# Optimization experiments

Measured on AMD Instinct MI355X. Metric: run time of the kernel, lower is better.

Reference implementation:

```python
import jax, jax.numpy as jnp
import numpy as np

N = 100000
E = 800000
D_IN, D_H, D_OUT = 128, 128, 128


def setup_inputs() -> dict:
    key = jax.random.key(0)
    ks = jax.random.split(key, 8)
    x = jax.random.normal(ks[0], (N, D_IN), dtype=jnp.float32)
    edge_index = jax.random.randint(ks[1], (2, E), 0, N, dtype=jnp.int64)
    s = 1.0 / np.sqrt(D_IN)
    W1 = jax.random.uniform(ks[2], (D_H, D_IN), minval=-s, maxval=s, dtype=jnp.float32)
    b1 = jax.random.uniform(ks[3], (D_H,), minval=-s, maxval=s, dtype=jnp.float32)
    sh = 1.0 / np.sqrt(D_H)
    W2 = jax.random.uniform(ks[4], (D_H, D_H), minval=-sh, maxval=sh, dtype=jnp.float32)
    b2 = jax.random.uniform(ks[5], (D_H,), minval=-sh, maxval=sh, dtype=jnp.float32)
    W3 = jax.random.uniform(ks[6], (D_OUT, D_H), minval=-sh, maxval=sh, dtype=jnp.float32)
    b3 = jax.random.uniform(ks[7], (D_OUT,), minval=-sh, maxval=sh, dtype=jnp.float32)
    return {"x": x, "edge_index": edge_index, "W1": W1, "b1": b1,
            "W2": W2, "b2": b2, "W3": W3, "b3": b3}


def reference(x, edge_index, W1, b1, W2, b2, W3, b3):
    row, col = edge_index[0], edge_index[1]
    n = x.shape[0]
    # in-degree of destination nodes (bincount over row), clamped to 1
    deg = jnp.clip(
        jax.ops.segment_sum(jnp.ones_like(row, dtype=x.dtype), row, num_segments=n),
        1.0)  # [N]

    def mp(h):
        # gather messages from source nodes, scatter-add to destinations, mean, relu
        agg = jax.ops.segment_sum(h[col], row, num_segments=n)  # [N, d]
        return jax.nn.relu(agg / deg[:, None])

    h = mp(x @ W1.T + b1)
    h = mp(h @ W2.T + b2)
    return h @ W3.T + b3
```

## Files before the change

kernel.cpp:

```cpp
#include <hip/hip_runtime.h>

#define NNODES 100000
#define NEDGES 800000
#define D 128
#define NB1 391


__global__ __launch_bounds__(256) void k_count(const int* __restrict__ ei,
                                               int* __restrict__ cnt) {
    int e = blockIdx.x * 256 + threadIdx.x;
    atomicAdd(&cnt[ei[e]], 1);
}

__global__ __launch_bounds__(256) void k_scan1(const int* __restrict__ cnt,
                                               int* __restrict__ off,
                                               int* __restrict__ bsum) {
    __shared__ int s[256];
    int t = threadIdx.x;
    int i = blockIdx.x * 256 + t;
    int v = (i < NNODES) ? cnt[i] : 0;
    s[t] = v;
    __syncthreads();
    for (int d = 1; d < 256; d <<= 1) {
        int a = (t >= d) ? s[t - d] : 0;
        __syncthreads();
        s[t] += a;
        __syncthreads();
    }
    if (i < NNODES) off[i] = s[t] - v;
    if (t == 255) bsum[blockIdx.x] = s[255];
}

__global__ __launch_bounds__(512) void k_scan2(int* __restrict__ bsum) {
    __shared__ int s[512];
    int t = threadIdx.x;
    int v = (t < NB1) ? bsum[t] : 0;
    s[t] = v;
    __syncthreads();
    for (int d = 1; d < 512; d <<= 1) {
        int a = (t >= d) ? s[t - d] : 0;
        __syncthreads();
        s[t] += a;
        __syncthreads();
    }
    if (t < NB1) bsum[t] = s[t] - v;
}

__global__ __launch_bounds__(256) void k_scan3(int* __restrict__ off,
                                               const int* __restrict__ bsum,
                                               int* __restrict__ cur) {
    int i = blockIdx.x * 256 + threadIdx.x;
    if (i < NNODES) {
        int o = off[i] + bsum[blockIdx.x];
        off[i] = o;
        cur[i] = o;
    }
}

__global__ __launch_bounds__(256) void k_fill(const int* __restrict__ ei,
                                              int* __restrict__ cur,
                                              int* __restrict__ csr) {
    int e = blockIdx.x * 256 + threadIdx.x;
    int r = ei[e];
    int c = ei[NEDGES + e];
    int p = atomicAdd(&cur[r], 1);
    csr[p] = c;
}


static __device__ __forceinline__ void fma4(float4& acc, float s, const float4& v) {
    acc.x = fmaf(s, v.x, acc.x);
    acc.y = fmaf(s, v.y, acc.y);
    acc.z = fmaf(s, v.z, acc.z);
    acc.w = fmaf(s, v.w, acc.w);
}

static __device__ __forceinline__ int swz(int j, int k) {
    return (k << 7) + ((((j >> 2) ^ (k & 31)) << 2) | (j & 3));
}

__global__ __launch_bounds__(512, 4) void k_gemm(const float* __restrict__ in,
                                                 const float* __restrict__ W,
                                                 const float* __restrict__ bias,
                                                 float* __restrict__ out) {
    __shared__ float Wt[D * D];
    int t = threadIdx.x;
#pragma unroll
    for (int it = 0; it < 8; ++it) {
        int e4 = it * 512 + t;
        float4 w = ((const float4*)W)[e4];
        int e = e4 * 4;
        int j = e >> 7, k = e & 127;
        Wt[swz(j, k + 0)] = w.x;
        Wt[swz(j, k + 1)] = w.y;
        Wt[swz(j, k + 2)] = w.z;
        Wt[swz(j, k + 3)] = w.w;
    }
    int jl = t & 31;
    int ng = t >> 5;
    int j0 = jl * 4;
    float4 b4 = *(const float4*)(bias + j0);
    __syncthreads();

    int nb = blockIdx.x * 64 + ng * 4;
    if (nb >= NNODES) return;
    const float* p0 = in + (size_t)(nb + 0) * D;
    const float* p1 = in + (size_t)(nb + 1) * D;
    const float* p2 = in + (size_t)(nb + 2) * D;
    const float* p3 = in + (size_t)(nb + 3) * D;
    float4 a0 = b4, a1 = b4, a2 = b4, a3 = b4;
#pragma unroll 4
    for (int k = 0; k < D; k += 4) {
        const float4 w0 = *(const float4*)(Wt + swz(j0, k + 0));
        const float4 w1 = *(const float4*)(Wt + swz(j0, k + 1));
        const float4 w2 = *(const float4*)(Wt + swz(j0, k + 2));
        const float4 w3 = *(const float4*)(Wt + swz(j0, k + 3));
        float4 x0 = *(const float4*)(p0 + k);
        float4 x1 = *(const float4*)(p1 + k);
        float4 x2 = *(const float4*)(p2 + k);
        float4 x3 = *(const float4*)(p3 + k);
        fma4(a0, x0.x, w0); fma4(a0, x0.y, w1); fma4(a0, x0.z, w2); fma4(a0, x0.w, w3);
        fma4(a1, x1.x, w0); fma4(a1, x1.y, w1); fma4(a1, x1.z, w2); fma4(a1, x1.w, w3);
        fma4(a2, x2.x, w0); fma4(a2, x2.y, w1); fma4(a2, x2.z, w2); fma4(a2, x2.w, w3);
        fma4(a3, x3.x, w0); fma4(a3, x3.y, w1); fma4(a3, x3.z, w2); fma4(a3, x3.w, w3);
    }
    *(float4*)(out + (size_t)(nb + 0) * D + j0) = a0;
    *(float4*)(out + (size_t)(nb + 1) * D + j0) = a1;
    *(float4*)(out + (size_t)(nb + 2) * D + j0) = a2;
    *(float4*)(out + (size_t)(nb + 3) * D + j0) = a3;
}


__global__ __launch_bounds__(256) void k_mp(const float* __restrict__ h,
                                            const int* __restrict__ off,
                                            const int* __restrict__ cnt,
                                            const int* __restrict__ csr,
                                            float* __restrict__ agg) {
    int gid = blockIdx.x * 256 + threadIdx.x;
    int node = gid >> 6;
    int lane = threadIdx.x & 63;
    if (node >= NNODES) return;
    int begin = off[node];
    int c = cnt[node];
    float ax = 0.f, ay = 0.f;
    for (int e = 0; e < c; ++e) {
        int src = csr[begin + e];
        float2 v = *(const float2*)(h + (size_t)src * D + lane * 2);
        ax += v.x;
        ay += v.y;
    }
    float inv = 1.0f / fmaxf((float)c, 1.0f);
    float2 r;
    r.x = fmaxf(ax * inv, 0.f);
    r.y = fmaxf(ay * inv, 0.f);
    *(float2*)(agg + (size_t)node * D + lane * 2) = r;
}


extern "C" void kernel_launch(void* const* d_in, const int* in_sizes, int n_in,
                              void* d_out, int out_size, void* d_ws, size_t ws_size,
                              hipStream_t stream) {
    const float* x  = (const float*)d_in[0];
    const int*   ei = (const int*)d_in[1];
    const float* W1 = (const float*)d_in[2];
    const float* b1 = (const float*)d_in[3];
    const float* W2 = (const float*)d_in[4];
    const float* b2 = (const float*)d_in[5];
    const float* W3 = (const float*)d_in[6];
    const float* b3 = (const float*)d_in[7];
    float* out = (float*)d_out;

    char* ws = (char*)d_ws;
    int* cnt  = (int*)(ws + 0);
    int* off  = (int*)(ws + (512 << 10));
    int* cur  = (int*)(ws + (1024 << 10));
    int* bsum = (int*)(ws + (1536 << 10));
    int* csr  = (int*)(ws + (2 << 20));
    float* A  = (float*)(ws + ((size_t)8 << 20));
    float* B  = (float*)(ws + ((size_t)64 << 20));

    hipMemsetAsync(cnt, 0, NNODES * sizeof(int), stream);
    k_count<<<NEDGES / 256, 256, 0, stream>>>(ei, cnt);
    k_scan1<<<NB1, 256, 0, stream>>>(cnt, off, bsum);
    k_scan2<<<1, 512, 0, stream>>>(bsum);
    k_scan3<<<NB1, 256, 0, stream>>>(off, bsum, cur);
    k_fill<<<NEDGES / 256, 256, 0, stream>>>(ei, cur, csr);

    int gemmGrid = (NNODES + 63) / 64;
    k_gemm<<<gemmGrid, 512, 0, stream>>>(x, W1, b1, A);
    k_mp<<<NNODES / 4, 256, 0, stream>>>(A, off, cnt, csr, B);
    k_gemm<<<gemmGrid, 512, 0, stream>>>(B, W2, b2, out);
    k_mp<<<NNODES / 4, 256, 0, stream>>>(out, off, cnt, csr, A);
    k_gemm<<<gemmGrid, 512, 0, stream>>>(A, W3, b3, out);
}
```

Baseline: 606.9 us.

## Pre-transpose weights, split GEMM output columns across blocks, unroll gather loop

Adds a small kernel that transposes each weight matrix into workspace. The GEMM then loads a 64-column half-tile into 32KB of shared memory with plain float4 copies instead of swizzled scalar stores. Each block now covers 128 nodes by 64 output columns, with occupancy raised to 8 blocks, meant to cut shared-memory footprint and per-block weight staging cost. The message-passing gather is unrolled by 4 so several row loads are in flight at once. The costs are three extra launches, input rows read twice (once per column half), and the loss of the bank-conflict swizzle.

```diff
diff --git a/kernel.cpp b/kernel.cpp
--- a/kernel.cpp
+++ b/kernel.cpp
@@ -68,6 +68,14 @@
 }
 
 
+__global__ __launch_bounds__(256) void k_tr(const float* __restrict__ W,
+                                            float* __restrict__ Wt) {
+    int i = blockIdx.x * 256 + threadIdx.x;
+    int j = i >> 7, k = i & 127;
+    Wt[k * D + j] = W[i];
+}
+
+
 static __device__ __forceinline__ void fma4(float4& acc, float s, const float4& v) {
     acc.x = fmaf(s, v.x, acc.x);
     acc.y = fmaf(s, v.y, acc.y);
@@ -75,34 +83,28 @@
     acc.w = fmaf(s, v.w, acc.w);
 }
 
-static __device__ __forceinline__ int swz(int j, int k) {
-    return (k << 7) + ((((j >> 2) ^ (k & 31)) << 2) | (j & 3));
-}
-
-__global__ __launch_bounds__(512, 4) void k_gemm(const float* __restrict__ in,
-                                                 const float* __restrict__ W,
+__global__ __launch_bounds__(512, 8) void k_gemm(const float* __restrict__ in,
+                                                 const float* __restrict__ Wt,
                                                  const float* __restrict__ bias,
                                                  float* __restrict__ out) {
-    __shared__ float Wt[D * D];
+    __shared__ float Ws[D * 64];
     int t = threadIdx.x;
+    int bh = blockIdx.x & 1;
+    int nblk = blockIdx.x >> 1;
+    const float4* Wg = (const float4*)Wt;
 #pragma unroll
-    for (int it = 0; it < 8; ++it) {
-        int e4 = it * 512 + t;
-        float4 w = ((const float4*)W)[e4];
-        int e = e4 * 4;
-        int j = e >> 7, k = e & 127;
-        Wt[swz(j, k + 0)] = w.x;
-        Wt[swz(j, k + 1)] = w.y;
-        Wt[swz(j, k + 2)] = w.z;
-        Wt[swz(j, k + 3)] = w.w;
-    }
-    int jl = t & 31;
-    int ng = t >> 5;
+    for (int it = 0; it < 4; ++it) {
+        int i4 = it * 512 + t;
+        int k = i4 >> 4, cg = i4 & 15;
+        ((float4*)Ws)[i4] = Wg[k * 32 + bh * 16 + cg];
+    }
+    int jl = t & 15;
+    int ng = t >> 4;
     int j0 = jl * 4;
-    float4 b4 = *(const float4*)(bias + j0);
+    float4 b4 = *(const float4*)(bias + bh * 64 + j0);
     __syncthreads();
 
-    int nb = blockIdx.x * 64 + ng * 4;
+    int nb = nblk * 128 + ng * 4;
     if (nb >= NNODES) return;
     const float* p0 = in + (size_t)(nb + 0) * D;
     const float* p1 = in + (size_t)(nb + 1) * D;
@@ -111,10 +113,10 @@
     float4 a0 = b4, a1 = b4, a2 = b4, a3 = b4;
 #pragma unroll 4
     for (int k = 0; k < D; k += 4) {
-        const float4 w0 = *(const float4*)(Wt + swz(j0, k + 0));
-        const float4 w1 = *(const float4*)(Wt + swz(j0, k + 1));
-        const float4 w2 = *(const float4*)(Wt + swz(j0, k + 2));
-        const float4 w3 = *(const float4*)(Wt + swz(j0, k + 3));
+        const float4 w0 = *(const float4*)(Ws + (k + 0) * 64 + j0);
+        const float4 w1 = *(const float4*)(Ws + (k + 1) * 64 + j0);
+        const float4 w2 = *(const float4*)(Ws + (k + 2) * 64 + j0);
+        const float4 w3 = *(const float4*)(Ws + (k + 3) * 64 + j0);
         float4 x0 = *(const float4*)(p0 + k);
         float4 x1 = *(const float4*)(p1 + k);
         float4 x2 = *(const float4*)(p2 + k);
@@ -124,10 +126,11 @@
         fma4(a2, x2.x, w0); fma4(a2, x2.y, w1); fma4(a2, x2.z, w2); fma4(a2, x2.w, w3);
         fma4(a3, x3.x, w0); fma4(a3, x3.y, w1); fma4(a3, x3.z, w2); fma4(a3, x3.w, w3);
     }
-    *(float4*)(out + (size_t)(nb + 0) * D + j0) = a0;
-    *(float4*)(out + (size_t)(nb + 1) * D + j0) = a1;
-    *(float4*)(out + (size_t)(nb + 2) * D + j0) = a2;
-    *(float4*)(out + (size_t)(nb + 3) * D + j0) = a3;
+    int jo = bh * 64 + j0;
+    *(float4*)(out + (size_t)(nb + 0) * D + jo) = a0;
+    *(float4*)(out + (size_t)(nb + 1) * D + jo) = a1;
+    *(float4*)(out + (size_t)(nb + 2) * D + jo) = a2;
+    *(float4*)(out + (size_t)(nb + 3) * D + jo) = a3;
 }
 
 
@@ -140,12 +143,25 @@
     int node = gid >> 6;
     int lane = threadIdx.x & 63;
     if (node >= NNODES) return;
-    int begin = off[node];
+    int b = off[node];
     int c = cnt[node];
     float ax = 0.f, ay = 0.f;
-    for (int e = 0; e < c; ++e) {
-        int src = csr[begin + e];
-        float2 v = *(const float2*)(h + (size_t)src * D + lane * 2);
+    int e = 0;
+    for (; e + 4 <= c; e += 4) {
+        int s0 = csr[b + e + 0];
+        int s1 = csr[b + e + 1];
+        int s2 = csr[b + e + 2];
+        int s3 = csr[b + e + 3];
+        float2 v0 = *(const float2*)(h + (size_t)s0 * D + lane * 2);
+        float2 v1 = *(const float2*)(h + (size_t)s1 * D + lane * 2);
+        float2 v2 = *(const float2*)(h + (size_t)s2 * D + lane * 2);
+        float2 v3 = *(const float2*)(h + (size_t)s3 * D + lane * 2);
+        ax += (v0.x + v1.x) + (v2.x + v3.x);
+        ay += (v0.y + v1.y) + (v2.y + v3.y);
+    }
+    for (; e < c; ++e) {
+        int s = csr[b + e];
+        float2 v = *(const float2*)(h + (size_t)s * D + lane * 2);
         ax += v.x;
         ay += v.y;
     }
@@ -176,20 +192,26 @@
     int* cur  = (int*)(ws + (1024 << 10));
     int* bsum = (int*)(ws + (1536 << 10));
     int* csr  = (int*)(ws + (2 << 20));
+    float* Wt1 = (float*)(ws + ((size_t)6 << 20));
+    float* Wt2 = (float*)(ws + ((size_t)6 << 20) + 65536);
+    float* Wt3 = (float*)(ws + ((size_t)6 << 20) + 131072);
     float* A  = (float*)(ws + ((size_t)8 << 20));
     float* B  = (float*)(ws + ((size_t)64 << 20));
 
     hipMemsetAsync(cnt, 0, NNODES * sizeof(int), stream);
+    k_tr<<<64, 256, 0, stream>>>(W1, Wt1);
+    k_tr<<<64, 256, 0, stream>>>(W2, Wt2);
+    k_tr<<<64, 256, 0, stream>>>(W3, Wt3);
     k_count<<<NEDGES / 256, 256, 0, stream>>>(ei, cnt);
     k_scan1<<<NB1, 256, 0, stream>>>(cnt, off, bsum);
     k_scan2<<<1, 512, 0, stream>>>(bsum);
     k_scan3<<<NB1, 256, 0, stream>>>(off, bsum, cur);
     k_fill<<<NEDGES / 256, 256, 0, stream>>>(ei, cur, csr);
 
-    int gemmGrid = (NNODES + 63) / 64;
-    k_gemm<<<gemmGrid, 512, 0, stream>>>(x, W1, b1, A);
+    int gemmGrid = 2 * ((NNODES + 127) / 128);
+    k_gemm<<<gemmGrid, 512, 0, stream>>>(x, Wt1, b1, A);
     k_mp<<<NNODES / 4, 256, 0, stream>>>(A, off, cnt, csr, B);
-    k_gemm<<<gemmGrid, 512, 0, stream>>>(B, W2, b2, out);
+    k_gemm<<<gemmGrid, 512, 0, stream>>>(B, Wt2, b2, out);
     k_mp<<<NNODES / 4, 256, 0, stream>>>(out, off, cnt, csr, A);
-    k_gemm<<<gemmGrid, 512, 0, stream>>>(A, W3, b3, out);
-}
+    k_gemm<<<gemmGrid, 512, 0, stream>>>(A, Wt3, b3, out);
+}
```

New measurement: 674.4 us. 1.11x slower.
